# Performance work log

Measured on AMD Instinct MI355X. Metric: run time of the kernel, lower is better.

The kernel has to match this reference:

```python
import jax, jax.numpy as jnp
import numpy as np

VOCAB = 100000
EMB = 128
B = 16384
C = 20
N = 20


def setup_inputs() -> dict:
    key = jax.random.key(0)
    k1, k2, k3, k4, k5 = jax.random.split(key, 5)
    initrange = 1.0 / EMB
    return {
        "pos_target": jax.random.randint(k1, (B,), 0, VOCAB),
        "pos_contexts": jax.random.randint(k2, (B, C), 0, VOCAB),
        "pos_negatives": jax.random.randint(k3, (B, N), 0, VOCAB),
        "context_table": jax.random.uniform(k4, (VOCAB, EMB), jnp.float32, -initrange, initrange),
        "output_table": jax.random.uniform(k5, (VOCAB, EMB), jnp.float32, -initrange, initrange),
    }


def reference(pos_target, pos_contexts, pos_negatives, context_table, output_table):
    # gather + sum over context window: [B, C, D] -> [B, D]
    mean_contexts = jnp.sum(context_table[pos_contexts], axis=1)
    emb_target = output_table[pos_target]           # [B, D]
    emb_negs = output_table[pos_negatives]          # [B, N, D]

    # positive objective: dot(mean_contexts, emb_target) per row
    pos_score = jnp.clip(jnp.sum(mean_contexts * emb_target, axis=1), -10.0, 10.0)
    objective = -jax.nn.log_sigmoid(pos_score)      # [B]

    # negative objective: bmm [B,N,D] x [B,D] -> [B,N]
    neg_score = jnp.clip(jnp.einsum("bnd,bd->bn", emb_negs, mean_contexts), -10.0, 10.0)
    neg_objective = -jnp.sum(jax.nn.log_sigmoid(-neg_score), axis=1)  # [B]

    return jnp.mean(objective + neg_objective)
```

## Files before the change

### kernel.cpp

```cpp
#include <hip/hip_runtime.h>
#include <math.h>

#define VOCAB 100000
#define EMB   128
#define BATCH 16384
#define CTX   20
#define NEG   20
#define NSCORE (NEG + 1)

__device__ __forceinline__ float fast_softplus(float x) {
    return __logf(1.0f + __expf(x));
}

__global__ __launch_bounds__(256, 4) void cbow_loss_kernel(
    const int*   __restrict__ pos_target,
    const int*   __restrict__ pos_contexts,
    const int*   __restrict__ pos_negatives,
    const float* __restrict__ context_table,
    const float* __restrict__ output_table,
    float*       __restrict__ out)
{
    const int tid  = threadIdx.x;
    const int lane = tid & 63;
    const int wave = tid >> 6;

    const int row = __builtin_amdgcn_readfirstlane(blockIdx.x * 4 + wave);

    const float2* ctab = (const float2*)context_table;
    const float2* otab = (const float2*)output_table;

    int cidx[CTX], sidx[NSCORE];
#pragma unroll
    for (int c = 0; c < CTX; ++c) cidx[c] = pos_contexts[row * CTX + c];
    sidx[0] = pos_target[row];
#pragma unroll
    for (int n = 0; n < NEG; ++n) sidx[1 + n] = pos_negatives[row * NEG + n];

    float2 cv[CTX];
    float2 sv[NSCORE];
#pragma unroll
    for (int c = 0; c < CTX; ++c) cv[c] = ctab[(size_t)cidx[c] * 64 + lane];
#pragma unroll
    for (int n = 0; n < NSCORE; ++n) sv[n] = otab[(size_t)sidx[n] * 64 + lane];

    float2 acc = make_float2(0.f, 0.f);
#pragma unroll
    for (int c = 0; c < CTX; ++c) { acc.x += cv[c].x; acc.y += cv[c].y; }

    float part[NSCORE];
#pragma unroll
    for (int n = 0; n < NSCORE; ++n)
        part[n] = fmaf(acc.x, sv[n].x, acc.y * sv[n].y);

#pragma unroll
    for (int s = 32; s >= 1; s >>= 1) {
#pragma unroll
        for (int n = 0; n < NSCORE; ++n) part[n] += __shfl_xor(part[n], s);
    }

    float ps = fminf(fmaxf(part[0], -10.f), 10.f);
    float loss = fast_softplus(-ps);
#pragma unroll
    for (int n = 1; n < NSCORE; ++n) {
        float ns = fminf(fmaxf(part[n], -10.f), 10.f);
        loss += fast_softplus(ns);
    }

    __shared__ float sdata[4];
    if (lane == 0) sdata[wave] = loss;
    __syncthreads();
    if (tid == 0) {
        float s = sdata[0] + sdata[1] + sdata[2] + sdata[3];
        atomicAdd(out, s * (1.0f / (float)BATCH));
    }
}

extern "C" void kernel_launch(void* const* d_in, const int* in_sizes, int n_in,
                              void* d_out, int out_size, void* d_ws, size_t ws_size,
                              hipStream_t stream) {
    const int*   pos_target    = (const int*)d_in[0];
    const int*   pos_contexts  = (const int*)d_in[1];
    const int*   pos_negatives = (const int*)d_in[2];
    const float* context_table = (const float*)d_in[3];
    const float* output_table  = (const float*)d_in[4];
    float* out = (float*)d_out;

    hipMemsetAsync(out, 0, sizeof(float), stream);

    const int rows_per_block = 4;
    const int grid = BATCH / rows_per_block;
    cbow_loss_kernel<<<grid, 256, 0, stream>>>(
        pos_target, pos_contexts, pos_negatives, context_table, output_table, out);
}
```

Measured before the change: 171.6 us.

## Stage embedding gathers directly into LDS and replace atomics with two-pass reduction

Each row now gets a single-wave block that issues 16-byte global_load_lds gathers of all 41 embedding rows into shared memory, two rows per instruction. Partial vmcnt waits let the context sum start while the output-table rows are still arriving. Dot-product reductions use DPP instead of shuffles, and the global atomicAdd plus memset are replaced by a per-row partial buffer and a separate reduce kernel. The aim is fewer registers per thread and wider, more memory-level-parallel gathers, at the cost of about 21 KB of LDS per one-wave block, which limits occupancy, and an extra kernel launch.

```diff
diff --git a/kernel.cpp b/kernel.cpp
--- a/kernel.cpp
+++ b/kernel.cpp
@@ -7,71 +7,102 @@
 #define CTX   20
 #define NEG   20
 #define NSCORE (NEG + 1)
+#define NROWS  (CTX + NSCORE)
+#define SLOTS  (NROWS + 1)
+
+#define AS3(p)  ((__attribute__((address_space(3))) void*)(p))
+#define AS1C(p) ((const __attribute__((address_space(1))) void*)(p))
 
 __device__ __forceinline__ float fast_softplus(float x) {
     return __logf(1.0f + __expf(x));
 }
 
-__global__ __launch_bounds__(256, 4) void cbow_loss_kernel(
+__device__ __forceinline__ float wave_sum_dpp(float x) {
+#define DPP_ADD(ctrl)                                                      \
+    x += __int_as_float(__builtin_amdgcn_update_dpp(                       \
+        0, __float_as_int(x), (ctrl), 0xf, 0xf, true));
+    DPP_ADD(0x111)
+    DPP_ADD(0x112)
+    DPP_ADD(0x114)
+    DPP_ADD(0x118)
+    DPP_ADD(0x142)
+    DPP_ADD(0x143)
+#undef DPP_ADD
+    return x;
+}
+
+__global__ __launch_bounds__(64) void cbow_stage_kernel(
     const int*   __restrict__ pos_target,
     const int*   __restrict__ pos_contexts,
     const int*   __restrict__ pos_negatives,
     const float* __restrict__ context_table,
     const float* __restrict__ output_table,
-    float*       __restrict__ out)
+    float*       __restrict__ partial)
 {
-    const int tid  = threadIdx.x;
-    const int lane = tid & 63;
-    const int wave = tid >> 6;
+    __shared__ __align__(1024) float smem[SLOTS * EMB];
+    const int lane = threadIdx.x;
+    const int row  = blockIdx.x;
 
-    const int row = __builtin_amdgcn_readfirstlane(blockIdx.x * 4 + wave);
+    int idx[SLOTS];
+#pragma unroll
+    for (int c = 0; c < CTX; ++c) idx[c] = pos_contexts[row * CTX + c];
+    idx[CTX] = pos_target[row];
+#pragma unroll
+    for (int n = 0; n < NEG; ++n) idx[CTX + 1 + n] = pos_negatives[row * NEG + n];
+    idx[NROWS] = idx[NROWS - 1];
 
-    const float2* ctab = (const float2*)context_table;
-    const float2* otab = (const float2*)output_table;
+#pragma unroll
+    for (int k = 0; k < 21; ++k) {
+        const char* tab = (2 * k < CTX) ? (const char*)context_table
+                                        : (const char*)output_table;
+        const long long ia = idx[2 * k];
+        const long long ib = idx[2 * k + 1];
+        const long long isel = (lane < 32) ? ia : ib;
+        const char* g = tab + isel * 512 + (long long)(lane & 31) * 16;
+        __builtin_amdgcn_global_load_lds(AS1C(g), AS3((char*)smem + k * 1024),
+                                         16, 0, 0);
+    }
 
-    int cidx[CTX], sidx[NSCORE];
-#pragma unroll
-    for (int c = 0; c < CTX; ++c) cidx[c] = pos_contexts[row * CTX + c];
-    sidx[0] = pos_target[row];
-#pragma unroll
-    for (int n = 0; n < NEG; ++n) sidx[1 + n] = pos_negatives[row * NEG + n];
-
-    float2 cv[CTX];
-    float2 sv[NSCORE];
-#pragma unroll
-    for (int c = 0; c < CTX; ++c) cv[c] = ctab[(size_t)cidx[c] * 64 + lane];
-#pragma unroll
-    for (int n = 0; n < NSCORE; ++n) sv[n] = otab[(size_t)sidx[n] * 64 + lane];
-
+    __asm__ volatile("s_waitcnt vmcnt(11)" ::: "memory");
+    const float2* sm2 = (const float2*)smem;
     float2 acc = make_float2(0.f, 0.f);
 #pragma unroll
-    for (int c = 0; c < CTX; ++c) { acc.x += cv[c].x; acc.y += cv[c].y; }
-
-    float part[NSCORE];
-#pragma unroll
-    for (int n = 0; n < NSCORE; ++n)
-        part[n] = fmaf(acc.x, sv[n].x, acc.y * sv[n].y);
-
-#pragma unroll
-    for (int s = 32; s >= 1; s >>= 1) {
-#pragma unroll
-        for (int n = 0; n < NSCORE; ++n) part[n] += __shfl_xor(part[n], s);
+    for (int c = 0; c < CTX; ++c) {
+        const float2 v = sm2[c * 64 + lane];
+        acc.x += v.x; acc.y += v.y;
     }
 
-    float ps = fminf(fmaxf(part[0], -10.f), 10.f);
-    float loss = fast_softplus(-ps);
+    __asm__ volatile("s_waitcnt vmcnt(0)" ::: "memory");
+    float loss = 0.f;
 #pragma unroll
-    for (int n = 1; n < NSCORE; ++n) {
-        float ns = fminf(fmaxf(part[n], -10.f), 10.f);
-        loss += fast_softplus(ns);
+    for (int n = 0; n < NSCORE; ++n) {
+        const float2 s = sm2[(CTX + n) * 64 + lane];
+        float p = fmaf(acc.x, s.x, acc.y * s.y);
+        float tot = wave_sum_dpp(p);
+        float sc = __shfl(tot, 63);
+        sc = fminf(fmaxf(sc, -10.f), 10.f);
+        loss += (n == 0) ? fast_softplus(-sc) : fast_softplus(sc);
     }
+    if (lane == 0) partial[row] = loss;
 
-    __shared__ float sdata[4];
-    if (lane == 0) sdata[wave] = loss;
+}
+
+__global__ __launch_bounds__(1024) void cbow_reduce_kernel(
+    const float* __restrict__ partial, float* __restrict__ out)
+{
+    const int tid = threadIdx.x;
+    float s = 0.f;
+#pragma unroll
+    for (int i = 0; i < BATCH / 1024; ++i) s += partial[tid + i * 1024];
+    s = wave_sum_dpp(s);
+    __shared__ float sw[16];
+    if ((tid & 63) == 63) sw[tid >> 6] = s;
     __syncthreads();
     if (tid == 0) {
-        float s = sdata[0] + sdata[1] + sdata[2] + sdata[3];
-        atomicAdd(out, s * (1.0f / (float)BATCH));
+        float t = 0.f;
+#pragma unroll
+        for (int i = 0; i < 16; ++i) t += sw[i];
+        out[0] = t * (1.0f / (float)BATCH);
     }
 }
 
@@ -83,12 +114,11 @@
     const int*   pos_negatives = (const int*)d_in[2];
     const float* context_table = (const float*)d_in[3];
     const float* output_table  = (const float*)d_in[4];
-    float* out = (float*)d_out;
+    float* out     = (float*)d_out;
+    float* partial = (float*)d_ws;
 
-    hipMemsetAsync(out, 0, sizeof(float), stream);
-
-    const int rows_per_block = 4;
-    const int grid = BATCH / rows_per_block;
-    cbow_loss_kernel<<<grid, 256, 0, stream>>>(
-        pos_target, pos_contexts, pos_negatives, context_table, output_table, out);
+    cbow_stage_kernel<<<BATCH, 64, 0, stream>>>(
+        pos_target, pos_contexts, pos_negatives, context_table, output_table,
+        partial);
+    cbow_reduce_kernel<<<1, 1024, 0, stream>>>(partial, out);
 }
```

After: 156.2 us. -9.0%, faster.
